# Optimization experiments

Measured on AMD Instinct MI355X. Metric: run time of the kernel, lower is better.

Reference implementation:

```python
import jax, jax.numpy as jnp
import numpy as np


def setup_inputs() -> dict:
    key = jax.random.key(0)
    k1, k2, k3 = jax.random.split(key, 3)
    B, Cin, H, W = 16, 128, 56, 56
    Cout, Kh, Kw = 256, 3, 3
    tensor = jax.random.normal(k1, (B, Cin, H, W), dtype=jnp.float32)
    weights = jax.random.normal(k2, (Cout, Cin, Kh, Kw), dtype=jnp.float32) * 0.05
    bias = jax.random.normal(k3, (Cout,), dtype=jnp.float32) * 0.05
    return {"tensor": tensor, "weights": weights, "bias": bias}


def reference(tensor, weights, bias):
    # OpticalConvolution: unfold (im2col) -> per-output-channel augmented dot
    # products (w . patch + b). Mathematically this is a standard 2D conv with
    # bias, expressed here as one fused conv instead of a per-channel loop.
    stride, padding, dilation = (1, 1), ((1, 1), (1, 1)), (1, 1)
    out = jax.lax.conv_general_dilated(
        tensor, weights,
        window_strides=stride,
        padding=padding,
        rhs_dilation=dilation,
        dimension_numbers=("NCHW", "OIHW", "NCHW"),
    )
    return out + bias[None, :, None, None]  # [B, Cout, H_out, W_out]
```

## Files before the change

kernel.cpp:

```cpp
#include <hip/hip_runtime.h>
#include <hip/hip_bf16.h>

typedef unsigned short ushort_t;
typedef unsigned int uint_t;

#define CIN   128
#define COUT  256
#define HH    56
#define WW    56
#define HWSZ  3136
#define BATCH 16
#define NPIX  50176
#define KTOT  1152

#define PROW_U 68
#define PATCH_U (4 * 58 * 68)

typedef __attribute__((ext_vector_type(8))) short bf16x8;
typedef __attribute__((ext_vector_type(4))) float f32x4;

__device__ __forceinline__ ushort_t f2bf(float v) {
    union { float f; uint_t u; } c; c.f = v;
    uint_t u = c.u;
    u += 0x7FFFu + ((u >> 16) & 1u);
    return (ushort_t)(u >> 16);
}

__device__ __forceinline__ uint_t pk2bf(float lo, float hi) {
    __hip_bfloat162 h = __float22bfloat162_rn(make_float2(lo, hi));
    union { __hip_bfloat162 h; uint_t u; } c; c.h = h;
    return c.u;
}

__global__ __launch_bounds__(256) void wprep(
    const float* __restrict__ weights, ushort_t* __restrict__ A2)
{
    __shared__ ushort_t lds_s[KTOT];
    const int tid = threadIdx.x;
    const int co  = blockIdx.x;
    const float* src = weights + (size_t)co * KTOT;
    #pragma unroll
    for (int k = 0; k < 5; ++k) {
        int idx = tid + k * 256;
        if (idx < KTOT) {
            int ci  = idx / 9;
            int pos = idx - ci * 9;
            lds_s[pos * 128 + ci] = f2bf(src[idx]);
        }
    }
    __syncthreads();
    int mt  = co >> 6;
    int ii  = (co >> 4) & 3;
    int l16 = co & 15;
    if (tid < 144) {
        int s    = tid >> 2;
        int quad = tid & 3;
        uint4 v = *(const uint4*)&lds_s[(s >> 2) * 128 + (s & 3) * 32 + quad * 8];
        *(uint4*)(A2 + ((size_t)((mt * 36 + s) * 4 + ii) * 64 + quad * 16 + l16) * 8) = v;
    }
}

__global__ __launch_bounds__(256, 2) void conv_direct(
    const ushort_t* __restrict__ A2,
    const float* __restrict__ tensor,
    const float* __restrict__ bias,
    float* __restrict__ out)
{
    __shared__ __align__(16) uint_t patch[PATCH_U];
    const int tid  = threadIdx.x;
    const int wave = tid >> 6;
    const int lane = tid & 63;
    const int quad = lane >> 4;
    const int l16  = lane & 15;

    const int bn = blockIdx.x;
    const int b  = bn / 28;
    const int y0 = (bn - b * 28) * 2;

    #pragma unroll
    for (int k = 0; k < 16; ++k) {
        int i4 = tid + k * 256;
        if (i4 < PATCH_U / 4) *(uint4*)&patch[i4 * 4] = make_uint4(0u, 0u, 0u, 0u);
    }
    __syncthreads();

    const float* src_b = tensor + (size_t)b * CIN * HWSZ;
    #pragma unroll
    for (int it = 0; it < 16; ++it) {
        int xq = tid & 15;
        int t2 = it * 16 + (tid >> 4);
        int cp = t2 & 63;
        int pr = t2 >> 6;
        int y  = y0 - 1 + pr;
        if (xq < 14 && (uint_t)y < (uint_t)HH) {
            const float* s0 = src_b + (size_t)(2 * cp) * HWSZ + y * WW + xq * 4;
            float4 va = *(const float4*)s0;
            float4 vb = *(const float4*)(s0 + HWSZ);
            uint_t* dst = &patch[(pr * 58 + xq * 4 + 1) * PROW_U + cp];
            dst[0 * PROW_U] = pk2bf(va.x, vb.x);
            dst[1 * PROW_U] = pk2bf(va.y, vb.y);
            dst[2 * PROW_U] = pk2bf(va.z, vb.z);
            dst[3 * PROW_U] = pk2bf(va.w, vb.w);
        }
    }
    __syncthreads();

    const ushort_t* patch_s = (const ushort_t*)patch;
    int bbase[7];
    #pragma unroll
    for (int j = 0; j < 7; ++j) {
        int p  = j * 16 + l16;
        int ro = p / 56;
        int x  = p - ro * 56;
        bbase[j] = (ro * 58 + x) * 136 + quad * 8;
    }

    const ushort_t* aPtr = A2 + ((size_t)(wave * 144) * 64 + lane) * 8;
    bf16x8 aCur[4], aNxt[4];
    #pragma unroll
    for (int i = 0; i < 4; ++i) aCur[i] = *(const bf16x8*)(aPtr + i * 512);

    const f32x4 zero = {0.f, 0.f, 0.f, 0.f};
    f32x4 acc[4][7];
    #pragma unroll
    for (int i = 0; i < 4; ++i)
        #pragma unroll
        for (int j = 0; j < 7; ++j) acc[i][j] = zero;

    #pragma unroll
    for (int pos = 0; pos < 9; ++pos) {
        const int dy = pos / 3 - 1;
        const int dx = pos % 3 - 1;
        const int poff = ((dy + 1) * 58 + (dx + 1)) * 136;
        #pragma unroll
        for (int cc = 0; cc < 4; ++cc) {
            const int s = pos * 4 + cc;
            if (s < 35) {
                aPtr += 2048;
                #pragma unroll
                for (int i = 0; i < 4; ++i)
                    aNxt[i] = *(const bf16x8*)(aPtr + i * 512);
            }
            bf16x8 bfr[7];
            #pragma unroll
            for (int j = 0; j < 7; ++j)
                bfr[j] = *(const bf16x8*)&patch_s[bbase[j] + poff + cc * 32];
            #pragma unroll
            for (int i = 0; i < 4; ++i)
                #pragma unroll
                for (int j = 0; j < 7; ++j)
                    acc[i][j] = __builtin_amdgcn_mfma_f32_16x16x32_bf16(
                        aCur[i], bfr[j], acc[i][j], 0, 0, 0);
            #pragma unroll
            for (int i = 0; i < 4; ++i) aCur[i] = aNxt[i];
        }
    }

    int opix[7];
    #pragma unroll
    for (int j = 0; j < 7; ++j) {
        int p  = j * 16 + l16;
        int ro = p / 56;
        int x  = p - ro * 56;
        opix[j] = (y0 + ro) * WW + x;
    }
    const size_t bout = (size_t)b * (COUT * HWSZ);
    #pragma unroll
    for (int i = 0; i < 4; ++i) {
        #pragma unroll
        for (int r = 0; r < 4; ++r) {
            int co = wave * 64 + i * 16 + quad * 4 + r;
            float bv = bias[co];
            size_t obase = bout + (size_t)co * HWSZ;
            #pragma unroll
            for (int j = 0; j < 7; ++j)
                out[obase + opix[j]] = acc[i][j][r] + bv;
        }
    }
}

__global__ void naive_conv(const float* __restrict__ in, const float* __restrict__ w,
                           const float* __restrict__ bias, float* __restrict__ out, int total) {
    int idx = blockIdx.x * 256 + threadIdx.x;
    if (idx >= total) return;
    int x = idx % WW; int t = idx / WW;
    int y = t % HH; t /= HH;
    int co = t % COUT; int b = t / COUT;
    float s = bias[co];
    const float* wr = w + (size_t)co * KTOT;
    for (int ci = 0; ci < CIN; ++ci) {
        const float* ir = in + (size_t)(b * CIN + ci) * HWSZ;
        for (int kh = 0; kh < 3; ++kh) {
            int yy = y + kh - 1;
            if ((uint_t)yy >= (uint_t)HH) continue;
            for (int kw = 0; kw < 3; ++kw) {
                int xx = x + kw - 1;
                if ((uint_t)xx >= (uint_t)WW) continue;
                s += ir[yy * WW + xx] * wr[ci * 9 + kh * 3 + kw];
            }
        }
    }
    out[idx] = s;
}

extern "C" void kernel_launch(void* const* d_in, const int* in_sizes, int n_in,
                              void* d_out, int out_size, void* d_ws, size_t ws_size,
                              hipStream_t stream) {
    const float* tensor  = (const float*)d_in[0];
    const float* weights = (const float*)d_in[1];
    const float* bias    = (const float*)d_in[2];
    float* out = (float*)d_out;

    const size_t A2_BYTES = (size_t)COUT * KTOT * 2;

    if (ws_size >= A2_BYTES) {
        ushort_t* A2 = (ushort_t*)d_ws;
        wprep<<<COUT, 256, 0, stream>>>(weights, A2);
        conv_direct<<<NPIX / 112, 256, 0, stream>>>(A2, tensor, bias, out);
    } else {
        int total = BATCH * COUT * HWSZ;
        naive_conv<<<(total + 255) / 256, 256, 0, stream>>>(tensor, weights, bias, out, total);
    }
}
```

Before: 110.6 us.

## Triple-buffer weight prefetch, zero only halo, remap blocks, raise MFMA priority

Replaces the full-patch zero fill and its barrier with zeroing only the halo columns and the boundary rows. Remaps block indices to interleave batch/row tiles, which may change L2 locality. Switches weight fragments from double to triple buffering so global loads are issued two steps ahead. Wraps the MFMA burst in s_setprio to favour matrix issue. This costs more registers, which may pressure occupancy at 2 blocks per CU.

Result: no change. 109.6 us (-0.9%).

```diff
diff --git a/kernel.cpp b/kernel.cpp
--- a/kernel.cpp
+++ b/kernel.cpp
@@ -73,16 +73,28 @@
     const int quad = lane >> 4;
     const int l16  = lane & 15;
 
-    const int bn = blockIdx.x;
-    const int b  = bn / 28;
-    const int y0 = (bn - b * 28) * 2;
-
-    #pragma unroll
-    for (int k = 0; k < 16; ++k) {
-        int i4 = tid + k * 256;
-        if (i4 < PATCH_U / 4) *(uint4*)&patch[i4 * 4] = make_uint4(0u, 0u, 0u, 0u);
-    }
-    __syncthreads();
+    const int bn0 = blockIdx.x;
+    const int bn  = (bn0 & 7) * 56 + (bn0 >> 3);
+    const int b   = bn / 28;
+    const int y0  = (bn - b * 28) * 2;
+
+    uint4* p4 = (uint4*)patch;
+    if (tid < 136) {
+        int pr   = tid / 34;
+        int r    = tid - pr * 34;
+        int side = r / 17;
+        int k    = r - side * 17;
+        int x    = side ? 57 : 0;
+        p4[(pr * 58 + x) * 17 + k] = make_uint4(0u, 0u, 0u, 0u);
+    }
+    if (y0 == 0) {
+        for (int g = tid; g < 952; g += 256)
+            p4[17 + g] = make_uint4(0u, 0u, 0u, 0u);
+    }
+    if (y0 == 54) {
+        for (int g = tid; g < 952; g += 256)
+            p4[2975 + g] = make_uint4(0u, 0u, 0u, 0u);
+    }
 
     const float* src_b = tensor + (size_t)b * CIN * HWSZ;
     #pragma unroll
@@ -115,10 +127,13 @@
         bbase[j] = (ro * 58 + x) * 136 + quad * 8;
     }
 
-    const ushort_t* aPtr = A2 + ((size_t)(wave * 144) * 64 + lane) * 8;
-    bf16x8 aCur[4], aNxt[4];
-    #pragma unroll
-    for (int i = 0; i < 4; ++i) aCur[i] = *(const bf16x8*)(aPtr + i * 512);
+    const ushort_t* aBase = A2 + ((size_t)(wave * 144) * 64 + lane) * 8;
+    bf16x8 aBuf[3][4];
+    #pragma unroll
+    for (int i = 0; i < 4; ++i) aBuf[0][i] = *(const bf16x8*)(aBase + i * 512);
+    #pragma unroll
+    for (int i = 0; i < 4; ++i) aBuf[1][i] = *(const bf16x8*)(aBase + 2048 + i * 512);
+    const ushort_t* aPtr = aBase + 2 * 2048;
 
     const f32x4 zero = {0.f, 0.f, 0.f, 0.f};
     f32x4 acc[4][7];
@@ -135,24 +150,24 @@
         #pragma unroll
         for (int cc = 0; cc < 4; ++cc) {
             const int s = pos * 4 + cc;
-            if (s < 35) {
-                aPtr += 2048;
+            if (s + 2 < 36) {
                 #pragma unroll
                 for (int i = 0; i < 4; ++i)
-                    aNxt[i] = *(const bf16x8*)(aPtr + i * 512);
+                    aBuf[(s + 2) % 3][i] = *(const bf16x8*)(aPtr + i * 512);
+                aPtr += 2048;
             }
             bf16x8 bfr[7];
             #pragma unroll
             for (int j = 0; j < 7; ++j)
                 bfr[j] = *(const bf16x8*)&patch_s[bbase[j] + poff + cc * 32];
+            __builtin_amdgcn_s_setprio(1);
             #pragma unroll
             for (int i = 0; i < 4; ++i)
                 #pragma unroll
                 for (int j = 0; j < 7; ++j)
                     acc[i][j] = __builtin_amdgcn_mfma_f32_16x16x32_bf16(
-                        aCur[i], bfr[j], acc[i][j], 0, 0, 0);
-            #pragma unroll
-            for (int i = 0; i < 4; ++i) aCur[i] = aNxt[i];
+                        aBuf[s % 3][i], bfr[j], acc[i][j], 0, 0, 0);
+            __builtin_amdgcn_s_setprio(0);
         }
     }
 
```
